# Kernel optimization log

Hardware: AMD Instinct MI355X
Metric: run time of the kernel (lower is better)

## Reference

```python
import jax, jax.numpy as jnp
import numpy as np

SCALE = 10000.0
EPS = 1e-5


def _extract_patches(x):
    # x: [B,28,28] int32 -> [B,28,28,9] (3x3 neighborhoods, zero-padded)
    xp = jnp.pad(x, ((0, 0), (1, 1), (1, 1)))
    ps = [xp[:, i:i + 28, j:j + 28] for i in range(3) for j in range(3)]
    return jnp.stack(ps, axis=-1)


def _bn_eval(x, g, b, m, v):
    inv = g / jnp.sqrt(v + EPS)
    return x * inv[None, :, None, None] + (b - m * inv)[None, :, None, None]


def _maxpool2(x):
    return jax.lax.reduce_window(x, -jnp.inf, jax.lax.max,
                                 (1, 1, 2, 2), (1, 1, 2, 2), 'VALID')


def _conv(x, w, b):
    y = jax.lax.conv_general_dilated(x, w, (1, 1), 'SAME',
                                     dimension_numbers=('NCHW', 'OIHW', 'NCHW'))
    return y + b[None, :, None, None]


def setup_inputs() -> dict:
    key = jax.random.key(0)
    ks = jax.random.split(key, 24)
    B = 1024
    inp = {}
    inp['x_img'] = jax.random.randint(ks[0], (B, 28, 28), 0, 256, dtype=jnp.int32)
    # quantized conv1 weights: round(w * 10000), signed
    inp['y_int'] = jax.random.randint(ks[1], (16, 9), 0, 20001, dtype=jnp.int32) - 10000
    inp['bias1'] = jax.random.normal(ks[2], (16,), jnp.float32)
    for i, (c, kg, kb, km, kv) in enumerate([(16, 3, 4, 5, 6), (32, 7, 8, 9, 10), (64, 11, 12, 13, 14)]):
        j = i + 1
        inp[f'g{j}'] = jax.random.uniform(ks[kg], (c,), jnp.float32, 0.5, 1.5)
        inp[f'b{j}'] = jax.random.normal(ks[kb], (c,), jnp.float32)
        inp[f'm{j}'] = jax.random.normal(ks[km], (c,), jnp.float32)
        inp[f'v{j}'] = jax.random.uniform(ks[kv], (c,), jnp.float32, 0.5, 1.5)
    inp['w2'] = jax.random.normal(ks[15], (32, 16, 3, 3), jnp.float32) * 0.1
    inp['bias2'] = jax.random.normal(ks[16], (32,), jnp.float32)
    inp['w3'] = jax.random.normal(ks[17], (64, 32, 3, 3), jnp.float32) * 0.1
    inp['bias3'] = jax.random.normal(ks[18], (64,), jnp.float32)
    inp['w_fc1'] = jax.random.normal(ks[19], (128, 576), jnp.float32) * 0.05
    inp['b_fc1'] = jax.random.normal(ks[20], (128,), jnp.float32)
    inp['w_fc2'] = jax.random.normal(ks[21], (10, 128), jnp.float32) * 0.1
    inp['b_fc2'] = jax.random.normal(ks[22], (10,), jnp.float32)
    return inp


def reference(x_img, y_int, bias1, g1, b1, m1, v1, w2, bias2, g2, b2, m2, v2,
              w3, bias3, g3, b3, m3, v3, w_fc1, b_fc1, w_fc2, b_fc2):
    # IPFE first conv: exact integer inner product <patch, y>, then /10000 + bias
    patches = _extract_patches(x_img)                      # [B,28,28,9] int32
    ip = jnp.einsum('bhwk,ok->bohw', patches, y_int)       # exact int32 dot
    feat = ip.astype(jnp.float32) / SCALE + bias1[None, :, None, None]  # [B,16,28,28]
    feat = _maxpool2(jax.nn.relu(_bn_eval(feat, g1, b1, m1, v1)))       # [B,16,14,14]
    feat = _maxpool2(jax.nn.relu(_bn_eval(_conv(feat, w2, bias2), g2, b2, m2, v2)))  # [B,32,7,7]
    feat = _maxpool2(jax.nn.relu(_bn_eval(_conv(feat, w3, bias3), g3, b3, m3, v3)))  # [B,64,3,3]
    flat = feat.reshape(feat.shape[0], -1)                 # [B,576]
    h = jax.nn.relu(flat @ w_fc1.T + b_fc1)                # [B,128] (dropout: eval mode)
    return h @ w_fc2.T + b_fc2                             # [B,10]
```

## Files before the change

### kernel.cpp

```cpp
#include <hip/hip_runtime.h>
#include <hip/hip_bf16.h>

#define EPS 1e-5f

typedef __attribute__((ext_vector_type(8))) short bf16x8;
typedef __attribute__((ext_vector_type(4))) float f32x4;
#define MFMA16(a, b, c) __builtin_amdgcn_mfma_f32_16x16x32_bf16(a, b, c, 0, 0, 0)

#define CST_OFF  144
#define W2F_H    1024
#define W3F_H    6144
#define WFC1F_H  24576
#define PREP_ITEMS (368 + 5120 + 18432 + 73728)

__device__ __forceinline__ unsigned short f2bf(float f) {
    unsigned int u = __builtin_bit_cast(unsigned int, f);
    return (unsigned short)((u + 0x7fffu + ((u >> 16) & 1u)) >> 16);
}

__global__ __launch_bounds__(256) void prep_kernel(
    const int* __restrict__ y_int,
    const float* __restrict__ w2, const float* __restrict__ w3,
    const float* __restrict__ wfc1,
    const float* __restrict__ bias1,
    const float* __restrict__ g1, const float* __restrict__ b1,
    const float* __restrict__ m1, const float* __restrict__ v1,
    const float* __restrict__ g2, const float* __restrict__ b2,
    const float* __restrict__ m2, const float* __restrict__ v2,
    const float* __restrict__ bias2,
    const float* __restrict__ g3, const float* __restrict__ b3,
    const float* __restrict__ m3, const float* __restrict__ v3,
    const float* __restrict__ bias3,
    float* __restrict__ ws)
{
    unsigned short* wsh = (unsigned short*)ws;
    int i = blockIdx.x * 256 + threadIdx.x;
    if (i < 144) {
        int k = i >> 4, c = i & 15;
        ws[i] = (float)y_int[c * 9 + k];
    } else if (i < 368) {
        int idx = i - 144;
        if (idx < 16) { int c = idx;
            ws[CST_OFF + idx] = g1[c] * rsqrtf(v1[c] + EPS) * 1e-4f;
        } else if (idx < 32) { int c = idx - 16;
            float inv = g1[c] * rsqrtf(v1[c] + EPS);
            ws[CST_OFF + idx] = bias1[c] * inv + b1[c] - m1[c] * inv;
        } else if (idx < 64) { int c = idx - 32;
            ws[CST_OFF + idx] = g2[c] * rsqrtf(v2[c] + EPS);
        } else if (idx < 96) { int c = idx - 64;
            float inv = g2[c] * rsqrtf(v2[c] + EPS);
            ws[CST_OFF + idx] = bias2[c] * inv + b2[c] - m2[c] * inv;
        } else if (idx < 160) { int c = idx - 96;
            ws[CST_OFF + idx] = g3[c] * rsqrtf(v3[c] + EPS);
        } else { int c = idx - 160;
            float inv = g3[c] * rsqrtf(v3[c] + EPS);
            ws[CST_OFF + idx] = bias3[c] * inv + b3[c] - m3[c] * inv;
        }
    } else {
        int e = i - 368;
        if (e < 5120) {
            int m = e / 2560, r = e % 2560, s = r >> 9, l = (r >> 3) & 63, j = e & 7;
            int kl  = ((l >> 4) << 3) + j;
            int tap = 2 * s + (kl >> 4), ci = kl & 15;
            int ch  = m * 16 + (l & 15);
            float v = (tap < 9) ? w2[ch * 144 + ci * 9 + tap] : 0.f;
            wsh[W2F_H + e] = f2bf(v);
        } else if (e < 5120 + 18432) {
            int e3 = e - 5120;
            int mt = e3 / 4608, r = e3 % 4608, ks = r >> 9, l = (r >> 3) & 63, j = e3 & 7;
            int ch = mt * 16 + (l & 15), ci = ((l >> 4) << 3) + j;
            wsh[W3F_H + e3] = f2bf(w3[ch * 288 + ci * 9 + ks]);
        } else {
            int ef = e - 23552;
            int mt = ef / 9216, r = ef % 9216, ks = r >> 9, l = (r >> 3) & 63, j = ef & 7;
            int ch = mt * 16 + (l & 15), k = ks * 32 + ((l >> 4) << 3) + j;
            wsh[WFC1F_H + ef] = f2bf(wfc1[ch * 576 + k]);
        }
    }
}

__global__ __launch_bounds__(256) void fused_cnn(
    const int* __restrict__ x_img,
    const float* __restrict__ ws,
    const float* __restrict__ bfc1,
    const float* __restrict__ wfc2, const float* __restrict__ bfc2,
    float* __restrict__ out)
{
    const int b    = blockIdx.x;
    const int tid  = threadIdx.x;
    const int lane = tid & 63;
    const int wv   = __builtin_amdgcn_readfirstlane(tid >> 6);
    const unsigned short* wsh = (const unsigned short*)ws;

    __shared__ __align__(16) float          s_img[900];
    __shared__ __align__(16) unsigned short s_f1h[4160];
    __shared__ __align__(16) unsigned short s_f2h[2592];
    __shared__ __align__(16) unsigned short s_flat[576];
    __shared__ __align__(16) float          s_h[128];
    __shared__ __align__(16) float          s_cst[224];

    const int* ximg = x_img + b * 784;
    for (int i = tid; i < 900; i += 256) {
        int r = i / 30, c = i % 30;
        float v = 0.f;
        if (r >= 1 && r <= 28 && c >= 1 && c <= 28)
            v = (float)ximg[(r - 1) * 28 + (c - 1)];
        s_img[i] = v;
    }
    for (int i = tid; i < 4160; i += 256) s_f1h[i] = 0;
    for (int i = tid; i < 2592; i += 256) s_f2h[i] = 0;
    if (tid < 224) s_cst[tid] = ws[CST_OFF + tid];
    __syncthreads();

    if (tid < 196) {
        int ph = tid / 14, pw = tid % 14;
        float acc[16][4];
        #pragma unroll
        for (int c = 0; c < 16; c++) {
            acc[c][0] = 0.f; acc[c][1] = 0.f; acc[c][2] = 0.f; acc[c][3] = 0.f;
        }
        const float* imgq = s_img + ph * 60 + pw * 2;
        #pragma unroll
        for (int k = 0; k < 9; k++) {
            const float* ip = imgq + (k / 3) * 30 + (k % 3);
            float x0 = ip[0], x1 = ip[1], x2 = ip[30], x3 = ip[31];
            const float4* yw = (const float4*)(ws + k * 16);
            float4 wA = yw[0], wB = yw[1], wC = yw[2], wD = yw[3];
            float wr[16] = {wA.x, wA.y, wA.z, wA.w, wB.x, wB.y, wB.z, wB.w,
                            wC.x, wC.y, wC.z, wC.w, wD.x, wD.y, wD.z, wD.w};
            #pragma unroll
            for (int c = 0; c < 16; c++) {
                float w = wr[c];
                acc[c][0] += w * x0; acc[c][1] += w * x1;
                acc[c][2] += w * x2; acc[c][3] += w * x3;
            }
        }
        unsigned int pk[8];
        #pragma unroll
        for (int c = 0; c < 16; c += 2) {
            float mx0 = fmaxf(fmaxf(acc[c][0], acc[c][1]), fmaxf(acc[c][2], acc[c][3]));
            float r0  = fmaxf(mx0 * s_cst[c] + s_cst[16 + c], 0.f);
            float mx1 = fmaxf(fmaxf(acc[c+1][0], acc[c+1][1]), fmaxf(acc[c+1][2], acc[c+1][3]));
            float r1  = fmaxf(mx1 * s_cst[c + 1] + s_cst[16 + c + 1], 0.f);
            pk[c >> 1] = (unsigned int)f2bf(r0) | ((unsigned int)f2bf(r1) << 16);
        }
        int pos = (ph + 1) * 16 + (pw + 1);
        *(uint4*)&s_f1h[pos * 16]     = make_uint4(pk[0], pk[1], pk[2], pk[3]);
        *(uint4*)&s_f1h[pos * 16 + 8] = make_uint4(pk[4], pk[5], pk[6], pk[7]);
    }
    __syncthreads();

    {
        const int m = wv & 1;
        const int x = lane & 15, half = lane >> 4;
        bf16x8 A2[5];
        #pragma unroll
        for (int s = 0; s < 5; s++)
            A2[s] = *(const bf16x8*)(const void*)(wsh + W2F_H + ((m * 5 + s) * 64 + lane) * 8);
        int voff[5];
        #pragma unroll
        for (int s = 0; s < 5; s++) {
            int tap = 2 * s + (half >> 1);
            int dy = (tap < 9) ? tap / 3 : 0, dx = (tap < 9) ? tap % 3 : 0;
            voff[s] = (dy * 16 + x + dx) * 32 + (half & 1) * 16;
        }
        const int ch0 = m * 16 + half * 4;
        float a2v[4], c2v[4];
        #pragma unroll
        for (int r = 0; r < 4; r++) { a2v[r] = s_cst[32 + ch0 + r]; c2v[r] = s_cst[64 + ch0 + r]; }

        int p0 = (wv < 2) ? 0 : 4, p1 = (wv < 2) ? 4 : 7;
        for (int p = p0; p < p1; p++) {
            const char* base = (const char*)s_f1h + p * 1024;
            f32x4 acc0 = {0.f, 0.f, 0.f, 0.f}, acc1 = {0.f, 0.f, 0.f, 0.f};
            #pragma unroll
            for (int s = 0; s < 5; s++) {
                bf16x8 b0 = *(const bf16x8*)(const void*)(base + voff[s]);
                bf16x8 b1 = *(const bf16x8*)(const void*)(base + 512 + voff[s]);
                acc0 = MFMA16(A2[s], b0, acc0);
                acc1 = MFMA16(A2[s], b1, acc1);
            }
            float hp[4];
            #pragma unroll
            for (int r = 0; r < 4; r++) {
                float vp = fmaxf(acc0[r], acc1[r]);
                hp[r] = fmaxf(vp, __shfl_xor(vp, 1));
            }
            if (!(x & 1) && x < 14) {
                int xp = x >> 1;
                unsigned int lo = (unsigned int)f2bf(fmaxf(hp[0] * a2v[0] + c2v[0], 0.f)) |
                                  ((unsigned int)f2bf(fmaxf(hp[1] * a2v[1] + c2v[1], 0.f)) << 16);
                unsigned int hi = (unsigned int)f2bf(fmaxf(hp[2] * a2v[2] + c2v[2], 0.f)) |
                                  ((unsigned int)f2bf(fmaxf(hp[3] * a2v[3] + c2v[3], 0.f)) << 16);
                *(uint2*)&s_f2h[((p + 1) * 9 + xp + 1) * 32 + ch0] = make_uint2(lo, hi);
            }
        }
    }
    __syncthreads();

    {
        const int mt = wv;
        const int x8 = lane & 7, ry = (lane >> 3) & 1, half = lane >> 4;
        bf16x8 A3[9];
        #pragma unroll
        for (int ks = 0; ks < 9; ks++)
            A3[ks] = *(const bf16x8*)(const void*)(wsh + W3F_H + ((mt * 9 + ks) * 64 + lane) * 8);
        int voff3[9];
        #pragma unroll
        for (int ks = 0; ks < 9; ks++) {
            int dy = ks / 3, dx = ks % 3;
            voff3[ks] = ((ry + dy) * 9 + x8 + dx) * 64 + half * 16;
        }
        const int ch0 = mt * 16 + half * 4;
        float a3v[4], c3v[4];
        #pragma unroll
        for (int r = 0; r < 4; r++) { a3v[r] = s_cst[96 + ch0 + r]; c3v[r] = s_cst[160 + ch0 + r]; }

        #pragma unroll
        for (int t = 0; t < 3; t++) {
            const char* base = (const char*)s_f2h + t * 1152;
            f32x4 acc = {0.f, 0.f, 0.f, 0.f};
            #pragma unroll
            for (int ks = 0; ks < 9; ks++) {
                bf16x8 bb = *(const bf16x8*)(const void*)(base + voff3[ks]);
                acc = MFMA16(A3[ks], bb, acc);
            }
            float hp[4];
            #pragma unroll
            for (int r = 0; r < 4; r++) {
                float vp = fmaxf(acc[r], __shfl_xor(acc[r], 8));
                hp[r] = fmaxf(vp, __shfl_xor(vp, 1));
            }
            if (ry == 0 && !(x8 & 1) && x8 < 6) {
                int xp = x8 >> 1;
                #pragma unroll
                for (int r = 0; r < 4; r++) {
                    float v = fmaxf(hp[r] * a3v[r] + c3v[r], 0.f);
                    s_flat[(ch0 + r) * 9 + t * 3 + xp] = f2bf(v);
                }
            }
        }
    }
    __syncthreads();

    {
        #pragma unroll
        for (int mi = 0; mi < 2; mi++) {
            int mt = wv + mi * 4;
            f32x4 acc = {0.f, 0.f, 0.f, 0.f};
            #pragma unroll
            for (int ks = 0; ks < 18; ks++) {
                bf16x8 a  = *(const bf16x8*)(const void*)(wsh + WFC1F_H + ((mt * 18 + ks) * 64 + lane) * 8);
                bf16x8 bb = *(const bf16x8*)(const void*)(&s_flat[ks * 32 + (lane >> 4) * 8]);
                acc = MFMA16(a, bb, acc);
            }
            if ((lane & 15) == 0) {
                int ch0 = mt * 16 + (lane >> 4) * 4;
                #pragma unroll
                for (int r = 0; r < 4; r++)
                    s_h[ch0 + r] = fmaxf(acc[r] + bfc1[ch0 + r], 0.f);
            }
        }
    }
    __syncthreads();

    if (tid < 160) {
        int o = tid / 16, l = tid % 16;
        float a = 0.f;
        #pragma unroll
        for (int k = l; k < 128; k += 16)
            a += s_h[k] * wfc2[o * 128 + k];
        a += __shfl_xor(a, 8);
        a += __shfl_xor(a, 4);
        a += __shfl_xor(a, 2);
        a += __shfl_xor(a, 1);
        if (l == 0) out[b * 10 + o] = a + bfc2[o];
    }
}

extern "C" void kernel_launch(void* const* d_in, const int* in_sizes, int n_in,
                              void* d_out, int out_size, void* d_ws, size_t ws_size,
                              hipStream_t stream) {
    float* ws = (float*)d_ws;
    prep_kernel<<<(PREP_ITEMS + 255) / 256, 256, 0, stream>>>(
        (const int*)d_in[1],
        (const float*)d_in[15],
        (const float*)d_in[17],
        (const float*)d_in[19],
        (const float*)d_in[2],
        (const float*)d_in[3], (const float*)d_in[4], (const float*)d_in[5], (const float*)d_in[6],
        (const float*)d_in[7], (const float*)d_in[8], (const float*)d_in[9], (const float*)d_in[10],
        (const float*)d_in[16],
        (const float*)d_in[11], (const float*)d_in[12], (const float*)d_in[13], (const float*)d_in[14],
        (const float*)d_in[18],
        ws);
    fused_cnn<<<1024, 256, 0, stream>>>(
        (const int*)d_in[0],
        ws,
        (const float*)d_in[20],
        (const float*)d_in[21], (const float*)d_in[22],
        (float*)d_out);
}
```

Baseline: 28.16 us.

## Process two images per block and share FC1 weight fragments across both

Each block now handles two images with 512 threads (8 waves), with every LDS buffer duplicated per image. The conv stages run four waves per image, and the FC1 stage packs both images into the MFMA N dimension so each weight fragment is loaded once for two images. Zero-fill is also vectorised to uint4 stores. This halves the block count and per-image FC1 weight traffic, but doubles LDS per block, which may limit occupancy. It also leaves 12 of the 16 MFMA columns unused in FC1.

```diff
diff --git a/kernel.cpp b/kernel.cpp
--- a/kernel.cpp
+++ b/kernel.cpp
@@ -79,7 +79,7 @@
     }
 }
 
-__global__ __launch_bounds__(256) void fused_cnn(
+__global__ __launch_bounds__(512, 4) void fused_cnn(
     const int* __restrict__ x_img,
     const float* __restrict__ ws,
     const float* __restrict__ bfc1,
@@ -90,68 +90,80 @@
     const int tid  = threadIdx.x;
     const int lane = tid & 63;
     const int wv   = __builtin_amdgcn_readfirstlane(tid >> 6);
+    const int img  = wv >> 2;
+    const int wv4  = wv & 3;
     const unsigned short* wsh = (const unsigned short*)ws;
 
-    __shared__ __align__(16) float          s_img[900];
-    __shared__ __align__(16) unsigned short s_f1h[4160];
-    __shared__ __align__(16) unsigned short s_f2h[2592];
-    __shared__ __align__(16) unsigned short s_flat[576];
-    __shared__ __align__(16) float          s_h[128];
+    __shared__ __align__(16) float          s_img[2][900];
+    __shared__ __align__(16) unsigned short s_f1h[2][4160];
+    __shared__ __align__(16) unsigned short s_f2h[2][2592];
+    __shared__ __align__(16) unsigned short s_flat[2][576];
+    __shared__ __align__(16) float          s_h[2][128];
     __shared__ __align__(16) float          s_cst[224];
 
-    const int* ximg = x_img + b * 784;
-    for (int i = tid; i < 900; i += 256) {
-        int r = i / 30, c = i % 30;
+    const int* ximg = x_img + (b * 2) * 784;
+    for (int i = tid; i < 1800; i += 512) {
+        int im = i / 900, p = i - im * 900;
+        int r = p / 30, c = p % 30;
         float v = 0.f;
         if (r >= 1 && r <= 28 && c >= 1 && c <= 28)
-            v = (float)ximg[(r - 1) * 28 + (c - 1)];
-        s_img[i] = v;
-    }
-    for (int i = tid; i < 4160; i += 256) s_f1h[i] = 0;
-    for (int i = tid; i < 2592; i += 256) s_f2h[i] = 0;
+            v = (float)ximg[im * 784 + (r - 1) * 28 + (c - 1)];
+        s_img[im][p] = v;
+    }
+    {
+        uint4 z = make_uint4(0u, 0u, 0u, 0u);
+        uint4* z1 = (uint4*)&s_f1h[0][0];
+        for (int i = tid; i < 1040; i += 512) z1[i] = z;
+        uint4* z2 = (uint4*)&s_f2h[0][0];
+        for (int i = tid; i < 648; i += 512) z2[i] = z;
+    }
     if (tid < 224) s_cst[tid] = ws[CST_OFF + tid];
     __syncthreads();
 
-    if (tid < 196) {
-        int ph = tid / 14, pw = tid % 14;
-        float acc[16][4];
-        #pragma unroll
-        for (int c = 0; c < 16; c++) {
-            acc[c][0] = 0.f; acc[c][1] = 0.f; acc[c][2] = 0.f; acc[c][3] = 0.f;
-        }
-        const float* imgq = s_img + ph * 60 + pw * 2;
-        #pragma unroll
-        for (int k = 0; k < 9; k++) {
-            const float* ip = imgq + (k / 3) * 30 + (k % 3);
-            float x0 = ip[0], x1 = ip[1], x2 = ip[30], x3 = ip[31];
-            const float4* yw = (const float4*)(ws + k * 16);
-            float4 wA = yw[0], wB = yw[1], wC = yw[2], wD = yw[3];
-            float wr[16] = {wA.x, wA.y, wA.z, wA.w, wB.x, wB.y, wB.z, wB.w,
-                            wC.x, wC.y, wC.z, wC.w, wD.x, wD.y, wD.z, wD.w};
+    {
+        const int t  = tid & 255;
+        const int ig = tid >> 8;
+        if (t < 196) {
+            int ph = t / 14, pw = t % 14;
+            float acc[16][4];
             #pragma unroll
             for (int c = 0; c < 16; c++) {
-                float w = wr[c];
-                acc[c][0] += w * x0; acc[c][1] += w * x1;
-                acc[c][2] += w * x2; acc[c][3] += w * x3;
-            }
-        }
-        unsigned int pk[8];
-        #pragma unroll
-        for (int c = 0; c < 16; c += 2) {
-            float mx0 = fmaxf(fmaxf(acc[c][0], acc[c][1]), fmaxf(acc[c][2], acc[c][3]));
-            float r0  = fmaxf(mx0 * s_cst[c] + s_cst[16 + c], 0.f);
-            float mx1 = fmaxf(fmaxf(acc[c+1][0], acc[c+1][1]), fmaxf(acc[c+1][2], acc[c+1][3]));
-            float r1  = fmaxf(mx1 * s_cst[c + 1] + s_cst[16 + c + 1], 0.f);
-            pk[c >> 1] = (unsigned int)f2bf(r0) | ((unsigned int)f2bf(r1) << 16);
-        }
-        int pos = (ph + 1) * 16 + (pw + 1);
-        *(uint4*)&s_f1h[pos * 16]     = make_uint4(pk[0], pk[1], pk[2], pk[3]);
-        *(uint4*)&s_f1h[pos * 16 + 8] = make_uint4(pk[4], pk[5], pk[6], pk[7]);
-    }
-    __syncthreads();
-
-    {
-        const int m = wv & 1;
+                acc[c][0] = 0.f; acc[c][1] = 0.f; acc[c][2] = 0.f; acc[c][3] = 0.f;
+            }
+            const float* imgq = &s_img[ig][0] + ph * 60 + pw * 2;
+            #pragma unroll
+            for (int k = 0; k < 9; k++) {
+                const float* ip = imgq + (k / 3) * 30 + (k % 3);
+                float x0 = ip[0], x1 = ip[1], x2 = ip[30], x3 = ip[31];
+                const float4* yw = (const float4*)(ws + k * 16);
+                float4 wA = yw[0], wB = yw[1], wC = yw[2], wD = yw[3];
+                float wr[16] = {wA.x, wA.y, wA.z, wA.w, wB.x, wB.y, wB.z, wB.w,
+                                wC.x, wC.y, wC.z, wC.w, wD.x, wD.y, wD.z, wD.w};
+                #pragma unroll
+                for (int c = 0; c < 16; c++) {
+                    float w = wr[c];
+                    acc[c][0] += w * x0; acc[c][1] += w * x1;
+                    acc[c][2] += w * x2; acc[c][3] += w * x3;
+                }
+            }
+            unsigned int pk[8];
+            #pragma unroll
+            for (int c = 0; c < 16; c += 2) {
+                float mx0 = fmaxf(fmaxf(acc[c][0], acc[c][1]), fmaxf(acc[c][2], acc[c][3]));
+                float r0  = fmaxf(mx0 * s_cst[c] + s_cst[16 + c], 0.f);
+                float mx1 = fmaxf(fmaxf(acc[c+1][0], acc[c+1][1]), fmaxf(acc[c+1][2], acc[c+1][3]));
+                float r1  = fmaxf(mx1 * s_cst[c + 1] + s_cst[16 + c + 1], 0.f);
+                pk[c >> 1] = (unsigned int)f2bf(r0) | ((unsigned int)f2bf(r1) << 16);
+            }
+            int pos = (ph + 1) * 16 + (pw + 1);
+            *(uint4*)&s_f1h[ig][pos * 16]     = make_uint4(pk[0], pk[1], pk[2], pk[3]);
+            *(uint4*)&s_f1h[ig][pos * 16 + 8] = make_uint4(pk[4], pk[5], pk[6], pk[7]);
+        }
+    }
+    __syncthreads();
+
+    {
+        const int m = wv4 & 1;
         const int x = lane & 15, half = lane >> 4;
         bf16x8 A2[5];
         #pragma unroll
@@ -169,9 +181,9 @@
         #pragma unroll
         for (int r = 0; r < 4; r++) { a2v[r] = s_cst[32 + ch0 + r]; c2v[r] = s_cst[64 + ch0 + r]; }
 
-        int p0 = (wv < 2) ? 0 : 4, p1 = (wv < 2) ? 4 : 7;
+        int p0 = (wv4 < 2) ? 0 : 4, p1 = (wv4 < 2) ? 4 : 7;
         for (int p = p0; p < p1; p++) {
-            const char* base = (const char*)s_f1h + p * 1024;
+            const char* base = (const char*)&s_f1h[img][0] + p * 1024;
             f32x4 acc0 = {0.f, 0.f, 0.f, 0.f}, acc1 = {0.f, 0.f, 0.f, 0.f};
             #pragma unroll
             for (int s = 0; s < 5; s++) {
@@ -192,14 +204,14 @@
                                   ((unsigned int)f2bf(fmaxf(hp[1] * a2v[1] + c2v[1], 0.f)) << 16);
                 unsigned int hi = (unsigned int)f2bf(fmaxf(hp[2] * a2v[2] + c2v[2], 0.f)) |
                                   ((unsigned int)f2bf(fmaxf(hp[3] * a2v[3] + c2v[3], 0.f)) << 16);
-                *(uint2*)&s_f2h[((p + 1) * 9 + xp + 1) * 32 + ch0] = make_uint2(lo, hi);
-            }
-        }
-    }
-    __syncthreads();
-
-    {
-        const int mt = wv;
+                *(uint2*)&s_f2h[img][((p + 1) * 9 + xp + 1) * 32 + ch0] = make_uint2(lo, hi);
+            }
+        }
+    }
+    __syncthreads();
+
+    {
+        const int mt = wv4;
         const int x8 = lane & 7, ry = (lane >> 3) & 1, half = lane >> 4;
         bf16x8 A3[9];
         #pragma unroll
@@ -218,7 +230,7 @@
 
         #pragma unroll
         for (int t = 0; t < 3; t++) {
-            const char* base = (const char*)s_f2h + t * 1152;
+            const char* base = (const char*)&s_f2h[img][0] + t * 1152;
             f32x4 acc = {0.f, 0.f, 0.f, 0.f};
             #pragma unroll
             for (int ks = 0; ks < 9; ks++) {
@@ -236,7 +248,7 @@
                 #pragma unroll
                 for (int r = 0; r < 4; r++) {
                     float v = fmaxf(hp[r] * a3v[r] + c3v[r], 0.f);
-                    s_flat[(ch0 + r) * 9 + t * 3 + xp] = f2bf(v);
+                    s_flat[img][(ch0 + r) * 9 + t * 3 + xp] = f2bf(v);
                 }
             }
         }
@@ -244,37 +256,36 @@
     __syncthreads();
 
     {
-        #pragma unroll
-        for (int mi = 0; mi < 2; mi++) {
-            int mt = wv + mi * 4;
-            f32x4 acc = {0.f, 0.f, 0.f, 0.f};
-            #pragma unroll
-            for (int ks = 0; ks < 18; ks++) {
-                bf16x8 a  = *(const bf16x8*)(const void*)(wsh + WFC1F_H + ((mt * 18 + ks) * 64 + lane) * 8);
-                bf16x8 bb = *(const bf16x8*)(const void*)(&s_flat[ks * 32 + (lane >> 4) * 8]);
-                acc = MFMA16(a, bb, acc);
-            }
-            if ((lane & 15) == 0) {
-                int ch0 = mt * 16 + (lane >> 4) * 4;
-                #pragma unroll
-                for (int r = 0; r < 4; r++)
-                    s_h[ch0 + r] = fmaxf(acc[r] + bfc1[ch0 + r], 0.f);
-            }
-        }
-    }
-    __syncthreads();
-
-    if (tid < 160) {
-        int o = tid / 16, l = tid % 16;
+        const int mt  = wv;
+        const int ib  = (lane >> 3) & 1;
+        f32x4 acc = {0.f, 0.f, 0.f, 0.f};
+        #pragma unroll
+        for (int ks = 0; ks < 18; ks++) {
+            bf16x8 a  = *(const bf16x8*)(const void*)(wsh + WFC1F_H + ((mt * 18 + ks) * 64 + lane) * 8);
+            bf16x8 bb = *(const bf16x8*)(const void*)(&s_flat[ib][ks * 32 + (lane >> 4) * 8]);
+            acc = MFMA16(a, bb, acc);
+        }
+        if ((lane & 7) == 0) {
+            int ch0 = mt * 16 + (lane >> 4) * 4;
+            #pragma unroll
+            for (int r = 0; r < 4; r++)
+                s_h[ib][ch0 + r] = fmaxf(acc[r] + bfc1[ch0 + r], 0.f);
+        }
+    }
+    __syncthreads();
+
+    if (tid < 320) {
+        int im = tid / 160, t = tid - im * 160;
+        int o = t / 16, l = t & 15;
         float a = 0.f;
         #pragma unroll
         for (int k = l; k < 128; k += 16)
-            a += s_h[k] * wfc2[o * 128 + k];
+            a += s_h[im][k] * wfc2[o * 128 + k];
         a += __shfl_xor(a, 8);
         a += __shfl_xor(a, 4);
         a += __shfl_xor(a, 2);
         a += __shfl_xor(a, 1);
-        if (l == 0) out[b * 10 + o] = a + bfc2[o];
+        if (l == 0) out[(b * 2 + im) * 10 + o] = a + bfc2[o];
     }
 }
 
@@ -294,7 +305,7 @@
         (const float*)d_in[11], (const float*)d_in[12], (const float*)d_in[13], (const float*)d_in[14],
         (const float*)d_in[18],
         ws);
-    fused_cnn<<<1024, 256, 0, stream>>>(
+    fused_cnn<<<512, 512, 0, stream>>>(
         (const int*)d_in[0],
         ws,
         (const float*)d_in[20],
```

New measurement: 27.46 us. 2.5% less time.

## Assign one image per wavefront and drop block-level barriers

Applied to the files above, without the earlier changes.

Each wavefront now processes a whole image independently, so four images share a block, the grid shrinks to 256 blocks, and all __syncthreads are removed. Shared memory is reorganized into per-wave regions with a channel-split layout for the feature maps, and conv2/conv3 weights are held in registers for all output tiles. The intent is to remove synchronization stalls and the imbalance from idle waves in each phase. The cost is heavy register pressure (36 conv3 fragments plus accumulators), large LDS use, and only 256 blocks on a 256-CU device, so occupancy and latency hiding are reduced.

```diff
diff --git a/kernel.cpp b/kernel.cpp
--- a/kernel.cpp
+++ b/kernel.cpp
@@ -5,6 +5,7 @@
 
 typedef __attribute__((ext_vector_type(8))) short bf16x8;
 typedef __attribute__((ext_vector_type(4))) float f32x4;
+typedef unsigned short ushort_t;
 #define MFMA16(a, b, c) __builtin_amdgcn_mfma_f32_16x16x32_bf16(a, b, c, 0, 0, 0)
 
 #define CST_OFF  144
@@ -79,202 +80,244 @@
     }
 }
 
-__global__ __launch_bounds__(256) void fused_cnn(
+__global__ __launch_bounds__(256, 1) void fused_cnn(
     const int* __restrict__ x_img,
     const float* __restrict__ ws,
     const float* __restrict__ bfc1,
     const float* __restrict__ wfc2, const float* __restrict__ bfc2,
     float* __restrict__ out)
 {
-    const int b    = blockIdx.x;
     const int tid  = threadIdx.x;
     const int lane = tid & 63;
     const int wv   = __builtin_amdgcn_readfirstlane(tid >> 6);
+    const int img  = blockIdx.x * 4 + wv;
     const unsigned short* wsh = (const unsigned short*)ws;
 
-    __shared__ __align__(16) float          s_img[900];
-    __shared__ __align__(16) unsigned short s_f1h[4160];
-    __shared__ __align__(16) unsigned short s_f2h[2592];
-    __shared__ __align__(16) unsigned short s_flat[576];
-    __shared__ __align__(16) float          s_h[128];
-    __shared__ __align__(16) float          s_cst[224];
-
-    const int* ximg = x_img + b * 784;
-    for (int i = tid; i < 900; i += 256) {
-        int r = i / 30, c = i % 30;
-        float v = 0.f;
-        if (r >= 1 && r <= 28 && c >= 1 && c <= 28)
-            v = (float)ximg[(r - 1) * 28 + (c - 1)];
-        s_img[i] = v;
-    }
-    for (int i = tid; i < 4160; i += 256) s_f1h[i] = 0;
-    for (int i = tid; i < 2592; i += 256) s_f2h[i] = 0;
-    if (tid < 224) s_cst[tid] = ws[CST_OFF + tid];
-    __syncthreads();
-
-    if (tid < 196) {
-        int ph = tid / 14, pw = tid % 14;
-        float acc[16][4];
-        #pragma unroll
-        for (int c = 0; c < 16; c++) {
-            acc[c][0] = 0.f; acc[c][1] = 0.f; acc[c][2] = 0.f; acc[c][3] = 0.f;
-        }
-        const float* imgq = s_img + ph * 60 + pw * 2;
-        #pragma unroll
-        for (int k = 0; k < 9; k++) {
-            const float* ip = imgq + (k / 3) * 30 + (k % 3);
-            float x0 = ip[0], x1 = ip[1], x2 = ip[30], x3 = ip[31];
-            const float4* yw = (const float4*)(ws + k * 16);
-            float4 wA = yw[0], wB = yw[1], wC = yw[2], wD = yw[3];
-            float wr[16] = {wA.x, wA.y, wA.z, wA.w, wB.x, wB.y, wB.z, wB.w,
-                            wC.x, wC.y, wC.z, wC.w, wD.x, wD.y, wD.z, wD.w};
+    __shared__ __align__(16) char s_all[53504];
+    char*  F1   = s_all + wv * 8192;
+    char*  F2   = s_all + 32768 + wv * 5184;
+    float* IMG  = (float*)F2;
+    ushort_t* FLAT = (ushort_t*)F1;
+    float* H    = (float*)(F1 + 1152);
+
+    #pragma unroll
+    for (int it = 0; it < 4; it++) {
+        int j = it * 64 + lane;
+        if (j < 225) ((float4*)IMG)[j] = make_float4(0.f, 0.f, 0.f, 0.f);
+    }
+    const int* xp = x_img + img * 784;
+    #pragma unroll
+    for (int it = 0; it < 13; it++) {
+        int j = it * 64 + lane;
+        if (j < 784) {
+            int r = j / 28, c = j - r * 28;
+            IMG[(r + 1) * 30 + (c + 1)] = (float)xp[j];
+        }
+    }
+    {
+        uint4 z = make_uint4(0u, 0u, 0u, 0u);
+        #pragma unroll
+        for (int it = 0; it < 8; it++) ((uint4*)F1)[it * 64 + lane] = z;
+    }
+
+    bf16x8 A2[2][5];
+    #pragma unroll
+    for (int m = 0; m < 2; m++)
+        #pragma unroll
+        for (int s = 0; s < 5; s++)
+            A2[m][s] = *(const bf16x8*)(const void*)(wsh + W2F_H + ((m * 5 + s) * 64 + lane) * 8);
+
+    #pragma unroll
+    for (int it = 0; it < 4; it++) {
+        int q = it * 64 + lane;
+        if (q < 196) {
+            int ph = q / 14, pw = q - ph * 14;
+            float acc[16][4];
             #pragma unroll
             for (int c = 0; c < 16; c++) {
-                float w = wr[c];
-                acc[c][0] += w * x0; acc[c][1] += w * x1;
-                acc[c][2] += w * x2; acc[c][3] += w * x3;
-            }
-        }
-        unsigned int pk[8];
-        #pragma unroll
-        for (int c = 0; c < 16; c += 2) {
-            float mx0 = fmaxf(fmaxf(acc[c][0], acc[c][1]), fmaxf(acc[c][2], acc[c][3]));
-            float r0  = fmaxf(mx0 * s_cst[c] + s_cst[16 + c], 0.f);
-            float mx1 = fmaxf(fmaxf(acc[c+1][0], acc[c+1][1]), fmaxf(acc[c+1][2], acc[c+1][3]));
-            float r1  = fmaxf(mx1 * s_cst[c + 1] + s_cst[16 + c + 1], 0.f);
-            pk[c >> 1] = (unsigned int)f2bf(r0) | ((unsigned int)f2bf(r1) << 16);
-        }
-        int pos = (ph + 1) * 16 + (pw + 1);
-        *(uint4*)&s_f1h[pos * 16]     = make_uint4(pk[0], pk[1], pk[2], pk[3]);
-        *(uint4*)&s_f1h[pos * 16 + 8] = make_uint4(pk[4], pk[5], pk[6], pk[7]);
-    }
-    __syncthreads();
-
-    {
-        const int m = wv & 1;
-        const int x = lane & 15, half = lane >> 4;
-        bf16x8 A2[5];
-        #pragma unroll
-        for (int s = 0; s < 5; s++)
-            A2[s] = *(const bf16x8*)(const void*)(wsh + W2F_H + ((m * 5 + s) * 64 + lane) * 8);
+                acc[c][0] = 0.f; acc[c][1] = 0.f; acc[c][2] = 0.f; acc[c][3] = 0.f;
+            }
+            const float* imgq = IMG + ph * 60 + pw * 2;
+            #pragma unroll
+            for (int k = 0; k < 9; k++) {
+                const float* ip = imgq + (k / 3) * 30 + (k % 3);
+                float x0 = ip[0], x1 = ip[1], x2 = ip[30], x3 = ip[31];
+                const float4* yw = (const float4*)(ws + k * 16);
+                float4 wA = yw[0], wB = yw[1], wC = yw[2], wD = yw[3];
+                float wr[16] = {wA.x, wA.y, wA.z, wA.w, wB.x, wB.y, wB.z, wB.w,
+                                wC.x, wC.y, wC.z, wC.w, wD.x, wD.y, wD.z, wD.w};
+                #pragma unroll
+                for (int c = 0; c < 16; c++) {
+                    float w = wr[c];
+                    acc[c][0] += w * x0; acc[c][1] += w * x1;
+                    acc[c][2] += w * x2; acc[c][3] += w * x3;
+                }
+            }
+            unsigned int pk[8];
+            #pragma unroll
+            for (int c = 0; c < 16; c += 2) {
+                float mx0 = fmaxf(fmaxf(acc[c][0], acc[c][1]), fmaxf(acc[c][2], acc[c][3]));
+                float r0  = fmaxf(mx0 * ws[CST_OFF + c] + ws[CST_OFF + 16 + c], 0.f);
+                float mx1 = fmaxf(fmaxf(acc[c+1][0], acc[c+1][1]), fmaxf(acc[c+1][2], acc[c+1][3]));
+                float r1  = fmaxf(mx1 * ws[CST_OFF + c + 1] + ws[CST_OFF + 16 + c + 1], 0.f);
+                pk[c >> 1] = (unsigned int)f2bf(r0) | ((unsigned int)f2bf(r1) << 16);
+            }
+            int pos = (ph + 1) * 16 + (pw + 1);
+            *(uint4*)(F1 + pos * 16)        = make_uint4(pk[0], pk[1], pk[2], pk[3]);
+            *(uint4*)(F1 + 4096 + pos * 16) = make_uint4(pk[4], pk[5], pk[6], pk[7]);
+        }
+    }
+
+    {
+        uint4 z = make_uint4(0u, 0u, 0u, 0u);
+        #pragma unroll
+        for (int it = 0; it < 6; it++) {
+            int j = it * 64 + lane;
+            if (j < 324) ((uint4*)F2)[j] = z;
+        }
+    }
+
+    {
+        const int x = lane & 15, g = lane >> 4;
+        const int t = g >> 1, c0 = g & 1;
         int voff[5];
         #pragma unroll
         for (int s = 0; s < 5; s++) {
-            int tap = 2 * s + (half >> 1);
+            int tap = 2 * s + t;
             int dy = (tap < 9) ? tap / 3 : 0, dx = (tap < 9) ? tap % 3 : 0;
-            voff[s] = (dy * 16 + x + dx) * 32 + (half & 1) * 16;
-        }
-        const int ch0 = m * 16 + half * 4;
-        float a2v[4], c2v[4];
-        #pragma unroll
-        for (int r = 0; r < 4; r++) { a2v[r] = s_cst[32 + ch0 + r]; c2v[r] = s_cst[64 + ch0 + r]; }
-
-        int p0 = (wv < 2) ? 0 : 4, p1 = (wv < 2) ? 4 : 7;
-        for (int p = p0; p < p1; p++) {
-            const char* base = (const char*)s_f1h + p * 1024;
-            f32x4 acc0 = {0.f, 0.f, 0.f, 0.f}, acc1 = {0.f, 0.f, 0.f, 0.f};
+            voff[s] = c0 * 4096 + (dy * 16 + x + dx) * 16;
+        }
+        float a2v[2][4], c2v[2][4];
+        #pragma unroll
+        for (int m = 0; m < 2; m++)
+            #pragma unroll
+            for (int r = 0; r < 4; r++) {
+                int ch = m * 16 + g * 4 + r;
+                a2v[m][r] = ws[CST_OFF + 32 + ch];
+                c2v[m][r] = ws[CST_OFF + 64 + ch];
+            }
+        for (int p = 0; p < 7; p++) {
+            const char* bp = F1 + p * 512;
+            bf16x8 B0[5], B1[5];
             #pragma unroll
             for (int s = 0; s < 5; s++) {
-                bf16x8 b0 = *(const bf16x8*)(const void*)(base + voff[s]);
-                bf16x8 b1 = *(const bf16x8*)(const void*)(base + 512 + voff[s]);
-                acc0 = MFMA16(A2[s], b0, acc0);
-                acc1 = MFMA16(A2[s], b1, acc1);
-            }
-            float hp[4];
-            #pragma unroll
-            for (int r = 0; r < 4; r++) {
-                float vp = fmaxf(acc0[r], acc1[r]);
-                hp[r] = fmaxf(vp, __shfl_xor(vp, 1));
-            }
-            if (!(x & 1) && x < 14) {
-                int xp = x >> 1;
-                unsigned int lo = (unsigned int)f2bf(fmaxf(hp[0] * a2v[0] + c2v[0], 0.f)) |
-                                  ((unsigned int)f2bf(fmaxf(hp[1] * a2v[1] + c2v[1], 0.f)) << 16);
-                unsigned int hi = (unsigned int)f2bf(fmaxf(hp[2] * a2v[2] + c2v[2], 0.f)) |
-                                  ((unsigned int)f2bf(fmaxf(hp[3] * a2v[3] + c2v[3], 0.f)) << 16);
-                *(uint2*)&s_f2h[((p + 1) * 9 + xp + 1) * 32 + ch0] = make_uint2(lo, hi);
-            }
-        }
-    }
-    __syncthreads();
-
-    {
-        const int mt = wv;
-        const int x8 = lane & 7, ry = (lane >> 3) & 1, half = lane >> 4;
-        bf16x8 A3[9];
-        #pragma unroll
-        for (int ks = 0; ks < 9; ks++)
-            A3[ks] = *(const bf16x8*)(const void*)(wsh + W3F_H + ((mt * 9 + ks) * 64 + lane) * 8);
+                B0[s] = *(const bf16x8*)(const void*)(bp + voff[s]);
+                B1[s] = *(const bf16x8*)(const void*)(bp + 256 + voff[s]);
+            }
+            #pragma unroll
+            for (int m = 0; m < 2; m++) {
+                f32x4 a0 = {0.f, 0.f, 0.f, 0.f}, a1 = {0.f, 0.f, 0.f, 0.f};
+                #pragma unroll
+                for (int s = 0; s < 5; s++) {
+                    a0 = MFMA16(A2[m][s], B0[s], a0);
+                    a1 = MFMA16(A2[m][s], B1[s], a1);
+                }
+                float hp[4];
+                #pragma unroll
+                for (int r = 0; r < 4; r++) {
+                    float vp = fmaxf(a0[r], a1[r]);
+                    hp[r] = fmaxf(vp, __shfl_xor(vp, 1));
+                }
+                if (!(x & 1) && x < 14) {
+                    int xp2 = x >> 1;
+                    int pp  = (p + 1) * 9 + xp2 + 1;
+                    int ch0 = m * 16 + g * 4;
+                    unsigned int lo = (unsigned int)f2bf(fmaxf(hp[0] * a2v[m][0] + c2v[m][0], 0.f)) |
+                                      ((unsigned int)f2bf(fmaxf(hp[1] * a2v[m][1] + c2v[m][1], 0.f)) << 16);
+                    unsigned int hi = (unsigned int)f2bf(fmaxf(hp[2] * a2v[m][2] + c2v[m][2], 0.f)) |
+                                      ((unsigned int)f2bf(fmaxf(hp[3] * a2v[m][3] + c2v[m][3], 0.f)) << 16);
+                    *(uint2*)(F2 + (ch0 >> 3) * 1296 + pp * 16 + (ch0 & 7) * 2) = make_uint2(lo, hi);
+                }
+            }
+        }
+    }
+
+    {
+        bf16x8 A3[36];
+        #pragma unroll
+        for (int f = 0; f < 36; f++)
+            A3[f] = *(const bf16x8*)(const void*)(wsh + W3F_H + (f * 64 + lane) * 8);
+        const int x8 = lane & 7, ry = (lane >> 3) & 1, qg = lane >> 4;
         int voff3[9];
         #pragma unroll
         for (int ks = 0; ks < 9; ks++) {
             int dy = ks / 3, dx = ks % 3;
-            voff3[ks] = ((ry + dy) * 9 + x8 + dx) * 64 + half * 16;
-        }
-        const int ch0 = mt * 16 + half * 4;
-        float a3v[4], c3v[4];
-        #pragma unroll
-        for (int r = 0; r < 4; r++) { a3v[r] = s_cst[96 + ch0 + r]; c3v[r] = s_cst[160 + ch0 + r]; }
-
+            voff3[ks] = qg * 1296 + ((ry + dy) * 9 + x8 + dx) * 16;
+        }
+        float a3v[4][4], c3v[4][4];
+        #pragma unroll
+        for (int mt = 0; mt < 4; mt++)
+            #pragma unroll
+            for (int r = 0; r < 4; r++) {
+                int ch = mt * 16 + qg * 4 + r;
+                a3v[mt][r] = ws[CST_OFF + 96 + ch];
+                c3v[mt][r] = ws[CST_OFF + 160 + ch];
+            }
         #pragma unroll
         for (int t = 0; t < 3; t++) {
-            const char* base = (const char*)s_f2h + t * 1152;
-            f32x4 acc = {0.f, 0.f, 0.f, 0.f};
-            #pragma unroll
-            for (int ks = 0; ks < 9; ks++) {
-                bf16x8 bb = *(const bf16x8*)(const void*)(base + voff3[ks]);
-                acc = MFMA16(A3[ks], bb, acc);
-            }
-            float hp[4];
-            #pragma unroll
-            for (int r = 0; r < 4; r++) {
-                float vp = fmaxf(acc[r], __shfl_xor(acc[r], 8));
-                hp[r] = fmaxf(vp, __shfl_xor(vp, 1));
-            }
-            if (ry == 0 && !(x8 & 1) && x8 < 6) {
-                int xp = x8 >> 1;
+            bf16x8 bb[9];
+            #pragma unroll
+            for (int ks = 0; ks < 9; ks++)
+                bb[ks] = *(const bf16x8*)(const void*)(F2 + t * 288 + voff3[ks]);
+            #pragma unroll
+            for (int mt = 0; mt < 4; mt++) {
+                f32x4 acc = {0.f, 0.f, 0.f, 0.f};
+                #pragma unroll
+                for (int ks = 0; ks < 9; ks++)
+                    acc = MFMA16(A3[mt * 9 + ks], bb[ks], acc);
+                float hp[4];
                 #pragma unroll
                 for (int r = 0; r < 4; r++) {
-                    float v = fmaxf(hp[r] * a3v[r] + c3v[r], 0.f);
-                    s_flat[(ch0 + r) * 9 + t * 3 + xp] = f2bf(v);
-                }
-            }
-        }
-    }
-    __syncthreads();
-
-    {
-        #pragma unroll
-        for (int mi = 0; mi < 2; mi++) {
-            int mt = wv + mi * 4;
+                    float vp = fmaxf(acc[r], __shfl_xor(acc[r], 8));
+                    hp[r] = fmaxf(vp, __shfl_xor(vp, 1));
+                }
+                if (ry == 0 && !(x8 & 1) && x8 < 6) {
+                    int xp3 = x8 >> 1;
+                    int ch0 = mt * 16 + qg * 4;
+                    #pragma unroll
+                    for (int r = 0; r < 4; r++) {
+                        float v = fmaxf(hp[r] * a3v[mt][r] + c3v[mt][r], 0.f);
+                        FLAT[(ch0 + r) * 9 + t * 3 + xp3] = f2bf(v);
+                    }
+                }
+            }
+        }
+    }
+
+    {
+        const int g = lane >> 4;
+        #pragma unroll
+        for (int mt = 0; mt < 8; mt++) {
             f32x4 acc = {0.f, 0.f, 0.f, 0.f};
             #pragma unroll
             for (int ks = 0; ks < 18; ks++) {
                 bf16x8 a  = *(const bf16x8*)(const void*)(wsh + WFC1F_H + ((mt * 18 + ks) * 64 + lane) * 8);
-                bf16x8 bb = *(const bf16x8*)(const void*)(&s_flat[ks * 32 + (lane >> 4) * 8]);
+                bf16x8 bb = *(const bf16x8*)(const void*)(FLAT + ks * 32 + g * 8);
                 acc = MFMA16(a, bb, acc);
             }
             if ((lane & 15) == 0) {
-                int ch0 = mt * 16 + (lane >> 4) * 4;
+                int ch0 = mt * 16 + g * 4;
                 #pragma unroll
                 for (int r = 0; r < 4; r++)
-                    s_h[ch0 + r] = fmaxf(acc[r] + bfc1[ch0 + r], 0.f);
-            }
-        }
-    }
-    __syncthreads();
-
-    if (tid < 160) {
-        int o = tid / 16, l = tid % 16;
-        float a = 0.f;
-        #pragma unroll
-        for (int k = l; k < 128; k += 16)
-            a += s_h[k] * wfc2[o * 128 + k];
-        a += __shfl_xor(a, 8);
-        a += __shfl_xor(a, 4);
-        a += __shfl_xor(a, 2);
-        a += __shfl_xor(a, 1);
-        if (l == 0) out[b * 10 + o] = a + bfc2[o];
+                    H[ch0 + r] = fmaxf(acc[r] + bfc1[ch0 + r], 0.f);
+            }
+        }
+    }
+
+    #pragma unroll
+    for (int it = 0; it < 2; it++) {
+        int idx = it * 64 + lane;
+        if (idx < 80) {
+            int o = idx >> 3, kk = idx & 7;
+            float a = 0.f;
+            #pragma unroll
+            for (int tt = 0; tt < 16; tt++)
+                a += H[kk + 8 * tt] * wfc2[o * 128 + kk + 8 * tt];
+            a += __shfl_xor(a, 4);
+            a += __shfl_xor(a, 2);
+            a += __shfl_xor(a, 1);
+            if ((lane & 7) == 0) out[img * 10 + o] = a + bfc2[o];
+        }
     }
 }
 
@@ -294,7 +337,7 @@
         (const float*)d_in[11], (const float*)d_in[12], (const float*)d_in[13], (const float*)d_in[14],
         (const float*)d_in[18],
         ws);
-    fused_cnn<<<1024, 256, 0, stream>>>(
+    fused_cnn<<<256, 256, 0, stream>>>(
         (const int*)d_in[0],
         ws,
         (const float*)d_in[20],
```

Result: slower. 46.43 us (+64.9%).
